# Optimization experiments

Hardware: AMD Instinct MI355X
Metric: run time of the kernel (lower is better)

The kernel has to match this reference:

```python
import jax, jax.numpy as jnp
import numpy as np

DIM = 256
NUM_HEADS = 8
HEAD_DIM = DIM // NUM_HEADS


def rope_sincos(H, W, head_dim, dtype=jnp.float32):
    n = head_dim // 4
    angle = 1.0 / (10000.0 ** jnp.linspace(0.0, 1.0, n))
    angle = jnp.repeat(angle, 2)  # (head_dim//2,)
    ph = jnp.arange(H, dtype=dtype)[:, None] * angle[None, :]  # (H, d/2)
    pw = jnp.arange(W, dtype=dtype)[:, None] * angle[None, :]  # (W, d/2)
    sin_h = jnp.broadcast_to(jnp.sin(ph)[:, None, :], (H, W, 2 * n))
    sin_w = jnp.broadcast_to(jnp.sin(pw)[None, :, :], (H, W, 2 * n))
    cos_h = jnp.broadcast_to(jnp.cos(ph)[:, None, :], (H, W, 2 * n))
    cos_w = jnp.broadcast_to(jnp.cos(pw)[None, :, :], (H, W, 2 * n))
    sin = jnp.concatenate([sin_h, sin_w], -1).reshape(H * W, head_dim)
    cos = jnp.concatenate([cos_h, cos_w], -1).reshape(H * W, head_dim)
    return sin, cos


def rotate_every_two(x):
    x1 = x[..., 0::2]
    x2 = x[..., 1::2]
    return jnp.stack([-x2, x1], axis=-1).reshape(x.shape)


def theta_shift(x, sin, cos):
    return x * cos + rotate_every_two(x) * sin


def conv1x1(x, w, b):
    # x: (B,C,H,W), w: (O,C,1,1)
    return jnp.einsum('bchw,oc->bohw', x, w[:, :, 0, 0]) + b[None, :, None, None]


def depthwise5x5(x, w, b):
    # x: (B,C,H,W), w: (C,1,5,5), groups=C
    y = jax.lax.conv_general_dilated(
        x, w, window_strides=(1, 1), padding=((2, 2), (2, 2)),
        feature_group_count=x.shape[1],
        dimension_numbers=('NCHW', 'OIHW', 'NCHW'))
    return y + b[None, :, None, None]


def setup_inputs() -> dict:
    key = jax.random.key(0)
    ks = jax.random.split(key, 7)
    B, C, H, W = 8, DIM, 64, 64
    x = jax.random.normal(ks[0], (B, C, H, W), dtype=jnp.float32)
    qkvo_w = 0.02 * jax.random.normal(ks[1], (4 * C, C, 1, 1), dtype=jnp.float32)
    qkvo_b = jnp.zeros((4 * C,), dtype=jnp.float32)
    lepe_w = 0.02 * jax.random.normal(ks[2], (C, 1, 5, 5), dtype=jnp.float32)
    lepe_b = jnp.zeros((C,), dtype=jnp.float32)
    proj_w = 0.02 * jax.random.normal(ks[3], (C, C, 1, 1), dtype=jnp.float32)
    proj_b = jnp.zeros((C,), dtype=jnp.float32)
    return {'x': x, 'qkvo_w': qkvo_w, 'qkvo_b': qkvo_b,
            'lepe_w': lepe_w, 'lepe_b': lepe_b,
            'proj_w': proj_w, 'proj_b': proj_b}


def reference(x, qkvo_w, qkvo_b, lepe_w, lepe_b, proj_w, proj_b):
    B, C, H, W = x.shape
    n, d = NUM_HEADS, HEAD_DIM
    L = H * W
    scale = d ** (-0.5)

    sin, cos = rope_sincos(H, W, d, dtype=x.dtype)  # (L, d)

    qkvo = conv1x1(x, qkvo_w, qkvo_b)          # (B, 4C, H, W)
    qkv = qkvo[:, :3 * C]                       # (B, 3C, H, W)
    o = qkvo[:, 3 * C:]                         # (B, C, H, W)
    lepe = depthwise5x5(qkv[:, 2 * C:], lepe_w, lepe_b)  # (B, C, H, W)

    # 'b (m n d) h w -> m b n (h w) d'
    qkv_r = qkv.reshape(B, 3, n, d, H * W).transpose(1, 0, 2, 4, 3)  # (3,B,n,L,d)
    q, k, v = qkv_r[0], qkv_r[1], qkv_r[2]

    q = jax.nn.elu(q) + 1.0
    k = jax.nn.elu(k) + 1.0

    kmean = k.mean(axis=2, keepdims=True)               # (B,n,1,d)
    z = jnp.einsum('bnld,bnmd->bnlm', q, kmean) * scale  # (B,n,L,1)

    q = theta_shift(q, sin, cos)
    k = theta_shift(k, sin, cos)

    c = (scale / L) ** 0.5
    kv = jnp.einsum('bnld,bnle->bnde', k * c, v * c)     # (B,n,d,d)
    vmean = v.mean(axis=2, keepdims=True)                # (B,n,1,d)

    res = jnp.einsum('bnld,bnde->bnle', q, kv) * (1.0 + 1.0 / (z + 1e-6)) - z * vmean
    # 'b n (h w) d -> b (n d) h w'
    res = res.reshape(B, n, H, W, d).transpose(0, 1, 4, 2, 3).reshape(B, C, H, W)
    res = res + lepe
    return conv1x1(res * o, proj_w, proj_b)
```

## Files before the change

kernel.cpp:

```cpp
#include <hip/hip_runtime.h>
#include <math.h>

typedef unsigned short u16;
typedef unsigned int u32;
typedef __attribute__((ext_vector_type(8))) short short8;
typedef __attribute__((ext_vector_type(4))) float f32x4;
typedef __attribute__((ext_vector_type(16))) float f32x16;

static constexpr float SCALE = 0.17677669529663687f;
static constexpr float C2    = 0.17677669529663687f / 4096.f;

__device__ __forceinline__ float bf2f(u16 u){
  union { u32 i; float f; } v; v.i = ((u32)u) << 16; return v.f;
}
__device__ __forceinline__ u16 f2bf(float f){
  union { float fl; u32 i; } v; v.fl = f;
  u32 r = v.i + 0x7fffu + ((v.i >> 16) & 1u);
  return (u16)(r >> 16);
}
__device__ __forceinline__ float eluP(float x){ return x > 0.f ? x + 1.f : __expf(x); }
__device__ __forceinline__ float rfreq(int j){
  const float t[8] = {1.f, 0.2682695795f, 0.0719685673f, 0.0193069773f,
                      0.0051794747f, 0.0013894955f, 0.0003727594f, 1e-4f};
  return t[j];
}
__device__ __forceinline__ void gload16(const u16* g, u16* l){
  __builtin_amdgcn_global_load_lds(
      (const __attribute__((address_space(1))) u32*)g,
      (__attribute__((address_space(3))) u32*)l, 16, 0, 0);
}

__global__ __launch_bounds__(256) void k_prep(
    const float* __restrict__ qw, const float* __restrict__ pw,
    u16* __restrict__ Whi, u16* __restrict__ Wlo,
    u16* __restrict__ Phi, u16* __restrict__ Plo)
{
  int idx = blockIdx.x * 256 + threadIdx.x;
  if (idx < 262144){
    float v = qw[idx]; u16 h = f2bf(v);
    Whi[idx] = h; Wlo[idx] = f2bf(v - bf2f(h));
  }
  if (idx < 65536){
    float v = pw[idx]; u16 h = f2bf(v);
    Phi[idx] = h; Plo[idx] = f2bf(v - bf2f(h));
  }
}

__global__ __launch_bounds__(256) void k_xt(
    const float* __restrict__ x, u16* __restrict__ XT)
{
  __shared__ float t[64][65];
  int l0 = blockIdx.x * 64, c0 = blockIdx.y * 64, b = blockIdx.z;
  const float* xp = x + (((long)b * 256 + c0) << 12) + l0;
  #pragma unroll
  for (int rep = 0; rep < 4; rep++){
    int idx = threadIdx.x + rep * 256;
    int r = idx >> 4, ch = (idx & 15) * 4;
    float4 f = *(const float4*)&xp[((long)r << 12) + ch];
    t[r][ch] = f.x; t[r][ch+1] = f.y; t[r][ch+2] = f.z; t[r][ch+3] = f.w;
  }
  __syncthreads();
  int r2 = threadIdx.x >> 2, c8 = (threadIdx.x & 3) * 16;
  u32 w[8];
  #pragma unroll
  for (int j = 0; j < 8; j++){
    float v0 = t[c8 + 2*j][r2], v1 = t[c8 + 2*j + 1][r2];
    w[j] = (u32)f2bf(v0) | ((u32)f2bf(v1) << 16);
  }
  long ob = (((long)b << 12) << 8) + ((long)(l0 + r2) << 8) + c0 + c8;
  *(uint4*)&XT[ob]     = make_uint4(w[0], w[1], w[2], w[3]);
  *(uint4*)&XT[ob + 8] = make_uint4(w[4], w[5], w[6], w[7]);
}

__global__ __launch_bounds__(256) void k_gemmA(
    const u16* __restrict__ Whi_, const u16* __restrict__ Wlo_,
    const u16* __restrict__ Bh_,
    const float* __restrict__ bias,
    u16* __restrict__ Q16, u16* __restrict__ K16,
    u16* __restrict__ V16, u16* __restrict__ O16,
    float* __restrict__ KMb, float* __restrict__ VMb)
{
  __shared__ __align__(16) u16 AhS[4096];
  __shared__ __align__(16) u16 AlS[4096];
  __shared__ __align__(16) u16 BhS[4096];
  __shared__ float scs[2][8][64];
  const int tid = threadIdx.x;
  const int nt = blockIdx.x, mt = blockIdx.y, b = blockIdx.z;
  const int m0 = mt * 128, n0 = nt * 128;
  const int wave = tid >> 6, lane = tid & 63;
  const int wm = wave & 1, wn = wave >> 1, qu = lane >> 4, ln = lane & 15;

  #pragma unroll
  for (int r = 0; r < 2; r++){
    int idx = tid + r * 256;
    int jj = idx >> 6, pp = idx & 63;
    float sn, cs; sincosf(rfreq(jj) * (float)pp, &sn, &cs);
    scs[0][jj][pp] = sn; scs[1][jj][pp] = cs;
  }

  const u16* bhp = Bh_ + (((long)b << 12) << 8);

  const int l4 = lane >> 2, c4 = lane & 3;
  const int gch = (c4 ^ (l4 & 3)) * 8;
  const int fch = (qu ^ (ln & 3)) * 8;

  f32x4 acc[4][4];
  #pragma unroll
  for (int im = 0; im < 4; im++)
    #pragma unroll
    for (int in = 0; in < 4; in++)
      #pragma unroll
      for (int r = 0; r < 4; r++) acc[im][in][r] = 0.f;

  for (int kk = 0; kk < 256; kk += 32){
    #pragma unroll
    for (int t = 0; t < 2; t++){
      int rw = wave * 32 + t * 16;
      int ga = (m0 + rw + l4) * 256 + kk + gch;
      long gb = (long)(n0 + rw + l4) * 256 + kk + gch;
      gload16(&Whi_[ga], &AhS[rw * 32]);
      gload16(&Wlo_[ga], &AlS[rw * 32]);
      gload16(&bhp[gb],  &BhS[rw * 32]);
    }
    __syncthreads();
    short8 fbh[4];
    #pragma unroll
    for (int in = 0; in < 4; in++){
      int row = wn * 64 + in * 16 + ln;
      fbh[in] = *(short8*)&BhS[row * 32 + fch];
    }
    #pragma unroll
    for (int im = 0; im < 4; im++){
      int row = wm * 64 + im * 16 + ln;
      short8 fah = *(short8*)&AhS[row * 32 + fch];
      short8 fal = *(short8*)&AlS[row * 32 + fch];
      #pragma unroll
      for (int in = 0; in < 4; in++){
        acc[im][in] = __builtin_amdgcn_mfma_f32_16x16x32_bf16(fah, fbh[in], acc[im][in], 0, 0, 0);
        acc[im][in] = __builtin_amdgcn_mfma_f32_16x16x32_bf16(fal, fbh[in], acc[im][in], 0, 0, 0);
      }
    }
    __syncthreads();
  }

  const int range = m0 >> 8;
  u16* dst = (range == 0) ? Q16 : (range == 1) ? K16 : (range == 2) ? V16 : O16;
  #pragma unroll
  for (int im = 0; im < 4; im++){
    const int mb = m0 + wm * 64 + im * 16 + qu * 4;
    float v[4][4];
    #pragma unroll
    for (int r = 0; r < 4; r++){
      float bia = bias[mb + r];
      #pragma unroll
      for (int in = 0; in < 4; in++){
        float t = acc[im][in][r] + bia;
        v[r][in] = (range < 2) ? eluP(t) : t;
      }
    }
    if (range == 1 || range == 2){
      float* mbuf = (range == 1) ? KMb : VMb;
      #pragma unroll
      for (int r = 0; r < 4; r++){
        float s = v[r][0] + v[r][1] + v[r][2] + v[r][3];
        s += __shfl_xor(s, 1); s += __shfl_xor(s, 2);
        s += __shfl_xor(s, 4); s += __shfl_xor(s, 8);
        if (ln == 0) atomicAdd(&mbuf[b * 256 + ((mb + r) & 255)], s);
      }
    }
    if (range == 1){
      const int p0 = (mb & 31) >> 1;
      #pragma unroll
      for (int half = 0; half < 2; half++){
        int p = p0 + half, j = p & 7;
        #pragma unroll
        for (int in = 0; in < 4; in++){
          int n = n0 + wn * 64 + in * 16 + ln;
          int pos = (p < 8) ? (n >> 6) : (n & 63);
          float sn = scs[0][j][pos], cs = scs[1][j][pos];
          float a = v[2*half][in], bb = v[2*half+1][in];
          v[2*half][in]   = a * cs - bb * sn;
          v[2*half+1][in] = bb * cs + a * sn;
        }
      }
    }
    #pragma unroll
    for (int r = 0; r < 4; r++){
      u16* rowp = dst + (((long)b * 256 + ((mb + r) & 255)) << 12);
      #pragma unroll
      for (int in = 0; in < 4; in++){
        int n = n0 + wn * 64 + in * 16 + ln;
        rowp[n] = f2bf(v[r][in]);
      }
    }
  }
}

__global__ __launch_bounds__(256) void k_kv(
    const u16* __restrict__ K16, const u16* __restrict__ V16, float* __restrict__ KVb)
{
  __shared__ float red[4][1024];
  const int n = blockIdx.x, b = blockIdx.y;
  const int tid = threadIdx.x, wave = tid >> 6, lane = tid & 63;
  const u16* kp = K16 + (((long)(b * 256 + n * 32)) << 12);
  const u16* vp = V16 + (((long)(b * 256 + n * 32)) << 12);
  const int m = lane & 31, kh = lane >> 5;
  const long row = ((long)m << 12);

  f32x16 acc;
  #pragma unroll
  for (int r = 0; r < 16; r++) acc[r] = 0.f;
  #pragma unroll 4
  for (int it = 0; it < 64; it++){
    int l = wave * 1024 + it * 16 + kh * 8;
    short8 a  = *(const short8*)&kp[row + l];
    short8 bf = *(const short8*)&vp[row + l];
    acc = __builtin_amdgcn_mfma_f32_32x32x16_bf16(a, bf, acc, 0, 0, 0);
  }
  #pragma unroll
  for (int reg = 0; reg < 16; reg++){
    int rr = (reg & 3) + 8 * (reg >> 2) + 4 * kh;
    red[wave][rr * 32 + m] = acc[reg];
  }
  __syncthreads();
  #pragma unroll
  for (int i = tid; i < 1024; i += 256){
    float s = red[0][i] + red[1][i] + red[2][i] + red[3][i];
    KVb[(((long)b * 8 + n) << 10) + i] = s * C2;
  }
}

__global__ __launch_bounds__(256) void k_lepe(
    const u16* __restrict__ V16, const float* __restrict__ lw,
    const float* __restrict__ lb, u16* __restrict__ Tb16)
{
  __shared__ float tile[20][68];
  __shared__ float wl[25];
  int ht = blockIdx.x, ch = blockIdx.y, b = blockIdx.z;
  int h0 = ht * 16;
  const u16* vp = V16 + (((long)b * 256 + ch) << 12);
  if (threadIdx.x < 25) wl[threadIdx.x] = lw[ch * 25 + threadIdx.x];
  for (int idx = threadIdx.x; idx < 20 * 68; idx += 256){
    int r = idx / 68, c = idx % 68;
    int gh = h0 + r - 2, gw = c - 2;
    float v = 0.f;
    if (gh >= 0 && gh < 64 && gw >= 0 && gw < 64) v = bf2f(vp[(gh << 6) + gw]);
    tile[r][c] = v;
  }
  __syncthreads();
  const float bia = lb[ch];
  #pragma unroll
  for (int r2 = 0; r2 < 4; r2++){
    int idx = threadIdx.x + r2 * 256;
    int oh = idx >> 6, ow = idx & 63;
    float s = bia;
    #pragma unroll
    for (int i = 0; i < 5; i++)
      #pragma unroll
      for (int j = 0; j < 5; j++) s += tile[oh + i][ow + j] * wl[i * 5 + j];
    Tb16[(((long)b * 256 + ch) << 12) + ((h0 + oh) << 6) + ow] = f2bf(s);
  }
}

__global__ __launch_bounds__(256) void k_res(
    const u16* __restrict__ Q16, const float* __restrict__ KMb,
    const float* __restrict__ KVb, const float* __restrict__ VMb,
    const u16* __restrict__ O16, const u16* __restrict__ Tb16,
    u16* __restrict__ TT16)
{
  __shared__ __align__(16) float kvs[1024];
  __shared__ float scs[2][8][64];
  __shared__ float kms[32], vms[32];
  const int b = blockIdx.z, n = blockIdx.y, tid = threadIdx.x;
  #pragma unroll
  for (int r = 0; r < 2; r++){
    int idx = tid + r * 256;
    int jj = idx >> 6, pp = idx & 63;
    float sn, cs; sincosf(rfreq(jj) * (float)pp, &sn, &cs);
    scs[0][jj][pp] = sn; scs[1][jj][pp] = cs;
  }
  {
    const float* kv = KVb + (((long)b * 8 + n) << 10);
    #pragma unroll
    for (int r = 0; r < 4; r++) kvs[tid + r * 256] = kv[tid + r * 256];
    if (tid < 32){
      kms[tid] = KMb[b * 256 + n * 32 + tid] * (1.f / 4096.f);
      vms[tid] = VMb[b * 256 + n * 32 + tid] * (1.f / 4096.f);
    }
  }
  __syncthreads();

  const int l = blockIdx.x * 256 + tid;
  const long cbase = ((long)(b * 256 + n * 32)) << 12;

  float q[32];
  #pragma unroll
  for (int d = 0; d < 32; d++) q[d] = bf2f(Q16[cbase + ((long)d << 12) + l]);
  float z = 0.f;
  #pragma unroll
  for (int d = 0; d < 32; d++) z += q[d] * kms[d];
  z *= SCALE;
  #pragma unroll
  for (int p = 0; p < 16; p++){
    int pos = (p < 8) ? (l >> 6) : (l & 63);
    float sn = scs[0][p & 7][pos], cs = scs[1][p & 7][pos];
    float q0 = q[2*p], q1 = q[2*p+1];
    q[2*p]   = q0 * cs - q1 * sn;
    q[2*p+1] = q1 * cs + q0 * sn;
  }

  float acc[32];
  #pragma unroll
  for (int e = 0; e < 32; e++) acc[e] = 0.f;
  #pragma unroll 8
  for (int d = 0; d < 32; d++){
    float qd = q[d];
    #pragma unroll
    for (int ec = 0; ec < 8; ec++){
      float4 kvv = *(float4*)&kvs[d * 32 + ec * 4];
      acc[ec*4+0] += qd * kvv.x;
      acc[ec*4+1] += qd * kvv.y;
      acc[ec*4+2] += qd * kvv.z;
      acc[ec*4+3] += qd * kvv.w;
    }
  }

  const float f = 1.f + 1.f / (z + 1e-6f);
  u32 w[16];
  #pragma unroll
  for (int e = 0; e < 32; e++){
    long off = cbase + ((long)e << 12) + l;
    float val = (acc[e] * f - z * vms[e] + bf2f(Tb16[off])) * bf2f(O16[off]);
    u16 h = f2bf(val);
    if (e & 1) w[e >> 1] |= ((u32)h << 16);
    else       w[e >> 1] = h;
  }
  long ob = (((long)b << 12) << 8) + ((long)l << 8) + n * 32;
  #pragma unroll
  for (int j = 0; j < 4; j++)
    *(uint4*)&TT16[ob + j * 8] = make_uint4(w[4*j], w[4*j+1], w[4*j+2], w[4*j+3]);
}

__global__ __launch_bounds__(256) void k_gemmP(
    const u16* __restrict__ Phi_, const u16* __restrict__ Plo_,
    const u16* __restrict__ TT16, const float* __restrict__ bias,
    float* __restrict__ out)
{
  __shared__ __align__(16) u16 AhS[4096];
  __shared__ __align__(16) u16 AlS[4096];
  __shared__ __align__(16) u16 BhS[4096];
  const int tid = threadIdx.x;
  const int nt = blockIdx.x, mt = blockIdx.y, b = blockIdx.z;
  const int m0 = mt * 128, n0 = nt * 128;
  const int wave = tid >> 6, lane = tid & 63;
  const int wm = wave & 1, wn = wave >> 1, qu = lane >> 4, ln = lane & 15;

  const u16* bhp = TT16 + (((long)b << 12) << 8);
  const int l4 = lane >> 2, c4 = lane & 3;
  const int gch = (c4 ^ (l4 & 3)) * 8;
  const int fch = (qu ^ (ln & 3)) * 8;

  f32x4 acc[4][4];
  #pragma unroll
  for (int im = 0; im < 4; im++)
    #pragma unroll
    for (int in = 0; in < 4; in++)
      #pragma unroll
      for (int r = 0; r < 4; r++) acc[im][in][r] = 0.f;

  for (int kk = 0; kk < 256; kk += 32){
    #pragma unroll
    for (int t = 0; t < 2; t++){
      int rw = wave * 32 + t * 16;
      int ga = (m0 + rw + l4) * 256 + kk + gch;
      long gb = (long)(n0 + rw + l4) * 256 + kk + gch;
      gload16(&Phi_[ga], &AhS[rw * 32]);
      gload16(&Plo_[ga], &AlS[rw * 32]);
      gload16(&bhp[gb],  &BhS[rw * 32]);
    }
    __syncthreads();
    short8 fbh[4];
    #pragma unroll
    for (int in = 0; in < 4; in++){
      int row = wn * 64 + in * 16 + ln;
      fbh[in] = *(short8*)&BhS[row * 32 + fch];
    }
    #pragma unroll
    for (int im = 0; im < 4; im++){
      int row = wm * 64 + im * 16 + ln;
      short8 fah = *(short8*)&AhS[row * 32 + fch];
      short8 fal = *(short8*)&AlS[row * 32 + fch];
      #pragma unroll
      for (int in = 0; in < 4; in++){
        acc[im][in] = __builtin_amdgcn_mfma_f32_16x16x32_bf16(fah, fbh[in], acc[im][in], 0, 0, 0);
        acc[im][in] = __builtin_amdgcn_mfma_f32_16x16x32_bf16(fal, fbh[in], acc[im][in], 0, 0, 0);
      }
    }
    __syncthreads();
  }
  #pragma unroll
  for (int im = 0; im < 4; im++){
    int mbase = m0 + wm * 64 + im * 16 + qu * 4;
    #pragma unroll
    for (int r = 0; r < 4; r++){
      int m = mbase + r;
      float bia = bias[m];
      float* row = out + (((long)b * 256 + m) << 12);
      #pragma unroll
      for (int in = 0; in < 4; in++){
        int n = n0 + wn * 64 + in * 16 + ln;
        row[n] = acc[im][in][r] + bia;
      }
    }
  }
}

extern "C" void kernel_launch(void* const* d_in, const int* in_sizes, int n_in,
                              void* d_out, int out_size, void* d_ws, size_t ws_size,
                              hipStream_t stream)
{
  const float* x  = (const float*)d_in[0];
  const float* qw = (const float*)d_in[1];
  const float* qb = (const float*)d_in[2];
  const float* lw = (const float*)d_in[3];
  const float* lb = (const float*)d_in[4];
  const float* pw = (const float*)d_in[5];
  const float* pb = (const float*)d_in[6];

  u16* W    = (u16*)d_ws;
  u16* Q16  = W;
  u16* K16  = Q16 + 8388608;
  u16* V16  = K16 + 8388608;
  u16* O16  = V16 + 8388608;
  u16* Tb16 = O16 + 8388608;
  u16* XT   = Tb16 + 8388608;
  u16* Whi  = XT + 8388608;
  u16* Wlo  = Whi + 262144;
  u16* Phi  = Wlo + 262144;
  u16* Plo  = Phi + 65536;
  float* KMb = (float*)(Plo + 65536);
  float* VMb = KMb + 2048;
  float* KVb = VMb + 2048;
  size_t total_bytes = (6ull*8388608 + 2*262144 + 2*65536) * 2 + (2048+2048+65536) * 4;
  if (ws_size < total_bytes) return;

  u16* TT16 = XT;

  hipMemsetAsync(KMb, 0, 4096 * 4, stream);
  k_prep<<<1024, 256, 0, stream>>>(qw, pw, Whi, Wlo, Phi, Plo);
  k_xt<<<dim3(64, 4, 8), 256, 0, stream>>>(x, XT);
  k_gemmA<<<dim3(32, 8, 8), 256, 0, stream>>>(Whi, Wlo, XT, qb,
                                              Q16, K16, V16, O16, KMb, VMb);
  k_kv<<<dim3(8, 8), 256, 0, stream>>>(K16, V16, KVb);
  k_lepe<<<dim3(4, 256, 8), 256, 0, stream>>>(V16, lw, lb, Tb16);
  k_res<<<dim3(16, 8, 8), 256, 0, stream>>>(Q16, KMb, KVb, VMb, O16, Tb16, TT16);
  k_gemmP<<<dim3(32, 2, 8), 256, 0, stream>>>(Phi, Plo, TT16, pb, (float*)d_out);
}
```

Before: 240.6 us.

## Merge prep/transpose and kv/lepe kernels, coalesce k_res stores via LDS

```diff
diff --git a/kernel.cpp b/kernel.cpp
--- a/kernel.cpp
+++ b/kernel.cpp
@@ -3,6 +3,7 @@
 
 typedef unsigned short u16;
 typedef unsigned int u32;
+typedef unsigned long long u64;
 typedef __attribute__((ext_vector_type(8))) short short8;
 typedef __attribute__((ext_vector_type(4))) float f32x4;
 typedef __attribute__((ext_vector_type(16))) float f32x16;
@@ -30,46 +31,49 @@
       (__attribute__((address_space(3))) u32*)l, 16, 0, 0);
 }
 
-__global__ __launch_bounds__(256) void k_prep(
-    const float* __restrict__ qw, const float* __restrict__ pw,
-    u16* __restrict__ Whi, u16* __restrict__ Wlo,
-    u16* __restrict__ Phi, u16* __restrict__ Plo)
-{
-  int idx = blockIdx.x * 256 + threadIdx.x;
-  if (idx < 262144){
-    float v = qw[idx]; u16 h = f2bf(v);
-    Whi[idx] = h; Wlo[idx] = f2bf(v - bf2f(h));
-  }
-  if (idx < 65536){
-    float v = pw[idx]; u16 h = f2bf(v);
-    Phi[idx] = h; Plo[idx] = f2bf(v - bf2f(h));
-  }
-}
-
-__global__ __launch_bounds__(256) void k_xt(
-    const float* __restrict__ x, u16* __restrict__ XT)
-{
-  __shared__ float t[64][65];
-  int l0 = blockIdx.x * 64, c0 = blockIdx.y * 64, b = blockIdx.z;
-  const float* xp = x + (((long)b * 256 + c0) << 12) + l0;
-  #pragma unroll
-  for (int rep = 0; rep < 4; rep++){
-    int idx = threadIdx.x + rep * 256;
-    int r = idx >> 4, ch = (idx & 15) * 4;
-    float4 f = *(const float4*)&xp[((long)r << 12) + ch];
-    t[r][ch] = f.x; t[r][ch+1] = f.y; t[r][ch+2] = f.z; t[r][ch+3] = f.w;
-  }
-  __syncthreads();
-  int r2 = threadIdx.x >> 2, c8 = (threadIdx.x & 3) * 16;
-  u32 w[8];
-  #pragma unroll
-  for (int j = 0; j < 8; j++){
-    float v0 = t[c8 + 2*j][r2], v1 = t[c8 + 2*j + 1][r2];
-    w[j] = (u32)f2bf(v0) | ((u32)f2bf(v1) << 16);
-  }
-  long ob = (((long)b << 12) << 8) + ((long)(l0 + r2) << 8) + c0 + c8;
-  *(uint4*)&XT[ob]     = make_uint4(w[0], w[1], w[2], w[3]);
-  *(uint4*)&XT[ob + 8] = make_uint4(w[4], w[5], w[6], w[7]);
+__global__ __launch_bounds__(256) void k_pre(
+    const float* __restrict__ x, const float* __restrict__ qw, const float* __restrict__ pw,
+    u16* __restrict__ XT, u16* __restrict__ Whi, u16* __restrict__ Wlo,
+    u16* __restrict__ Phi, u16* __restrict__ Plo, float* __restrict__ KM0)
+{
+  if (blockIdx.z < 8){
+    __shared__ float t[64][65];
+    int l0 = blockIdx.x * 64, c0 = blockIdx.y * 64, b = blockIdx.z;
+    const float* xp = x + (((long)b * 256 + c0) << 12) + l0;
+    #pragma unroll
+    for (int rep = 0; rep < 4; rep++){
+      int idx = threadIdx.x + rep * 256;
+      int r = idx >> 4, ch = (idx & 15) * 4;
+      float4 f = *(const float4*)&xp[((long)r << 12) + ch];
+      t[r][ch] = f.x; t[r][ch+1] = f.y; t[r][ch+2] = f.z; t[r][ch+3] = f.w;
+    }
+    __syncthreads();
+    int r2 = threadIdx.x >> 2, c8 = (threadIdx.x & 3) * 16;
+    u32 w[8];
+    #pragma unroll
+    for (int j = 0; j < 8; j++){
+      float v0 = t[c8 + 2*j][r2], v1 = t[c8 + 2*j + 1][r2];
+      w[j] = (u32)f2bf(v0) | ((u32)f2bf(v1) << 16);
+    }
+    long ob = (((long)b << 12) << 8) + ((long)(l0 + r2) << 8) + c0 + c8;
+    *(uint4*)&XT[ob]     = make_uint4(w[0], w[1], w[2], w[3]);
+    *(uint4*)&XT[ob + 8] = make_uint4(w[4], w[5], w[6], w[7]);
+  } else {
+    int bid = (blockIdx.z - 8) * 256 + blockIdx.y * 64 + blockIdx.x;
+    int idx = bid * 256 + threadIdx.x;
+    if (idx < 262144){
+      float v = qw[idx]; u16 h = f2bf(v);
+      Whi[idx] = h; Wlo[idx] = f2bf(v - bf2f(h));
+    }
+    if (idx < 65536){
+      float v = pw[idx]; u16 h = f2bf(v);
+      Phi[idx] = h; Plo[idx] = f2bf(v - bf2f(h));
+    }
+    if (bid == 0){
+      #pragma unroll
+      for (int i = 0; i < 16; i++) KM0[threadIdx.x + i * 256] = 0.f;
+    }
+  }
 }
 
 __global__ __launch_bounds__(256) void k_gemmA(
@@ -196,69 +200,69 @@
   }
 }
 
-__global__ __launch_bounds__(256) void k_kv(
-    const u16* __restrict__ K16, const u16* __restrict__ V16, float* __restrict__ KVb)
-{
-  __shared__ float red[4][1024];
-  const int n = blockIdx.x, b = blockIdx.y;
-  const int tid = threadIdx.x, wave = tid >> 6, lane = tid & 63;
-  const u16* kp = K16 + (((long)(b * 256 + n * 32)) << 12);
-  const u16* vp = V16 + (((long)(b * 256 + n * 32)) << 12);
-  const int m = lane & 31, kh = lane >> 5;
-  const long row = ((long)m << 12);
-
-  f32x16 acc;
-  #pragma unroll
-  for (int r = 0; r < 16; r++) acc[r] = 0.f;
-  #pragma unroll 4
-  for (int it = 0; it < 64; it++){
-    int l = wave * 1024 + it * 16 + kh * 8;
-    short8 a  = *(const short8*)&kp[row + l];
-    short8 bf = *(const short8*)&vp[row + l];
-    acc = __builtin_amdgcn_mfma_f32_32x32x16_bf16(a, bf, acc, 0, 0, 0);
-  }
-  #pragma unroll
-  for (int reg = 0; reg < 16; reg++){
-    int rr = (reg & 3) + 8 * (reg >> 2) + 4 * kh;
-    red[wave][rr * 32 + m] = acc[reg];
-  }
-  __syncthreads();
-  #pragma unroll
-  for (int i = tid; i < 1024; i += 256){
-    float s = red[0][i] + red[1][i] + red[2][i] + red[3][i];
-    KVb[(((long)b * 8 + n) << 10) + i] = s * C2;
-  }
-}
-
-__global__ __launch_bounds__(256) void k_lepe(
-    const u16* __restrict__ V16, const float* __restrict__ lw,
-    const float* __restrict__ lb, u16* __restrict__ Tb16)
-{
-  __shared__ float tile[20][68];
-  __shared__ float wl[25];
-  int ht = blockIdx.x, ch = blockIdx.y, b = blockIdx.z;
-  int h0 = ht * 16;
-  const u16* vp = V16 + (((long)b * 256 + ch) << 12);
-  if (threadIdx.x < 25) wl[threadIdx.x] = lw[ch * 25 + threadIdx.x];
-  for (int idx = threadIdx.x; idx < 20 * 68; idx += 256){
-    int r = idx / 68, c = idx % 68;
-    int gh = h0 + r - 2, gw = c - 2;
-    float v = 0.f;
-    if (gh >= 0 && gh < 64 && gw >= 0 && gw < 64) v = bf2f(vp[(gh << 6) + gw]);
-    tile[r][c] = v;
-  }
-  __syncthreads();
-  const float bia = lb[ch];
-  #pragma unroll
-  for (int r2 = 0; r2 < 4; r2++){
-    int idx = threadIdx.x + r2 * 256;
-    int oh = idx >> 6, ow = idx & 63;
-    float s = bia;
-    #pragma unroll
-    for (int i = 0; i < 5; i++)
-      #pragma unroll
-      for (int j = 0; j < 5; j++) s += tile[oh + i][ow + j] * wl[i * 5 + j];
-    Tb16[(((long)b * 256 + ch) << 12) + ((h0 + oh) << 6) + ow] = f2bf(s);
+__global__ __launch_bounds__(256) void k_mid(
+    const u16* __restrict__ K16, const u16* __restrict__ V16,
+    const float* __restrict__ lw, const float* __restrict__ lb,
+    u16* __restrict__ Tb16, float* __restrict__ KVb)
+{
+  if (blockIdx.y < 256){
+    __shared__ float tile[20][68];
+    __shared__ float wl[25];
+    int ht = blockIdx.x, ch = blockIdx.y, b = blockIdx.z;
+    int h0 = ht * 16;
+    const u16* vp = V16 + (((long)b * 256 + ch) << 12);
+    if (threadIdx.x < 25) wl[threadIdx.x] = lw[ch * 25 + threadIdx.x];
+    for (int idx = threadIdx.x; idx < 20 * 68; idx += 256){
+      int r = idx / 68, c = idx % 68;
+      int gh = h0 + r - 2, gw = c - 2;
+      float v = 0.f;
+      if (gh >= 0 && gh < 64 && gw >= 0 && gw < 64) v = bf2f(vp[(gh << 6) + gw]);
+      tile[r][c] = v;
+    }
+    __syncthreads();
+    const float bia = lb[ch];
+    #pragma unroll
+    for (int r2 = 0; r2 < 4; r2++){
+      int idx = threadIdx.x + r2 * 256;
+      int oh = idx >> 6, ow = idx & 63;
+      float s = bia;
+      #pragma unroll
+      for (int i = 0; i < 5; i++)
+        #pragma unroll
+        for (int j = 0; j < 5; j++) s += tile[oh + i][ow + j] * wl[i * 5 + j];
+      Tb16[(((long)b * 256 + ch) << 12) + ((h0 + oh) << 6) + ow] = f2bf(s);
+    }
+  } else {
+    __shared__ float red[4][1024];
+    int kvIdx = (blockIdx.y - 256) * 32 + blockIdx.z * 4 + blockIdx.x;
+    int n = kvIdx & 7, b = kvIdx >> 3;
+    const int tid = threadIdx.x, wave = tid >> 6, lane = tid & 63;
+    const u16* kp = K16 + (((long)(b * 256 + n * 32)) << 12);
+    const u16* vp = V16 + (((long)(b * 256 + n * 32)) << 12);
+    const int m = lane & 31, kh = lane >> 5;
+    const long row = ((long)m << 12);
+
+    f32x16 acc;
+    #pragma unroll
+    for (int r = 0; r < 16; r++) acc[r] = 0.f;
+    #pragma unroll 4
+    for (int it = 0; it < 64; it++){
+      int l = wave * 1024 + it * 16 + kh * 8;
+      short8 a  = *(const short8*)&kp[row + l];
+      short8 bf = *(const short8*)&vp[row + l];
+      acc = __builtin_amdgcn_mfma_f32_32x32x16_bf16(a, bf, acc, 0, 0, 0);
+    }
+    #pragma unroll
+    for (int reg = 0; reg < 16; reg++){
+      int rr = (reg & 3) + 8 * (reg >> 2) + 4 * kh;
+      red[wave][rr * 32 + m] = acc[reg];
+    }
+    __syncthreads();
+    #pragma unroll
+    for (int i = tid; i < 1024; i += 256){
+      float s = red[0][i] + red[1][i] + red[2][i] + red[3][i];
+      KVb[(((long)b * 8 + n) << 10) + i] = s * C2;
+    }
   }
 }
 
@@ -271,6 +275,7 @@
   __shared__ __align__(16) float kvs[1024];
   __shared__ float scs[2][8][64];
   __shared__ float kms[32], vms[32];
+  __shared__ __align__(16) u64 tts[256 * 9];
   const int b = blockIdx.z, n = blockIdx.y, tid = threadIdx.x;
   #pragma unroll
   for (int r = 0; r < 2; r++){
@@ -290,7 +295,8 @@
   }
   __syncthreads();
 
-  const int l = blockIdx.x * 256 + tid;
+  const int l0 = blockIdx.x * 256;
+  const int l = l0 + tid;
   const long cbase = ((long)(b * 256 + n * 32)) << 12;
 
   float q[32];
@@ -335,10 +341,19 @@
     if (e & 1) w[e >> 1] |= ((u32)h << 16);
     else       w[e >> 1] = h;
   }
-  long ob = (((long)b << 12) << 8) + ((long)l << 8) + n * 32;
-  #pragma unroll
-  for (int j = 0; j < 4; j++)
-    *(uint4*)&TT16[ob + j * 8] = make_uint4(w[4*j], w[4*j+1], w[4*j+2], w[4*j+3]);
+  #pragma unroll
+  for (int j = 0; j < 8; j++)
+    tts[tid * 9 + j] = (u64)w[2*j] | ((u64)w[2*j+1] << 32);
+  __syncthreads();
+  #pragma unroll
+  for (int it = 0; it < 4; it++){
+    int row = (tid >> 2) + 64 * it;
+    int cc = tid & 3;
+    u64 a  = tts[row * 9 + cc * 2];
+    u64 bb = tts[row * 9 + cc * 2 + 1];
+    long orow = (((long)b << 12) << 8) + ((long)(l0 + row) << 8) + n * 32 + cc * 8;
+    *(uint4*)&TT16[orow] = make_uint4((u32)a, (u32)(a >> 32), (u32)bb, (u32)(bb >> 32));
+  }
 }
 
 __global__ __launch_bounds__(256) void k_gemmP(
@@ -446,13 +461,10 @@
 
   u16* TT16 = XT;
 
-  hipMemsetAsync(KMb, 0, 4096 * 4, stream);
-  k_prep<<<1024, 256, 0, stream>>>(qw, pw, Whi, Wlo, Phi, Plo);
-  k_xt<<<dim3(64, 4, 8), 256, 0, stream>>>(x, XT);
+  k_pre<<<dim3(64, 4, 12), 256, 0, stream>>>(x, qw, pw, XT, Whi, Wlo, Phi, Plo, KMb);
   k_gemmA<<<dim3(32, 8, 8), 256, 0, stream>>>(Whi, Wlo, XT, qb,
                                               Q16, K16, V16, O16, KMb, VMb);
-  k_kv<<<dim3(8, 8), 256, 0, stream>>>(K16, V16, KVb);
-  k_lepe<<<dim3(4, 256, 8), 256, 0, stream>>>(V16, lw, lb, Tb16);
+  k_mid<<<dim3(4, 258, 8), 256, 0, stream>>>(K16, V16, lw, lb, Tb16, KVb);
   k_res<<<dim3(16, 8, 8), 256, 0, stream>>>(Q16, KMb, KVb, VMb, O16, Tb16, TT16);
   k_gemmP<<<dim3(32, 2, 8), 256, 0, stream>>>(Phi, Plo, TT16, pb, (float*)d_out);
 }
```

New measurement: 233.8 us. 2.8% less time.
